# Performance work log

Measured on AMD Instinct MI355X. Metric: run time of the kernel, lower is better.

Reference implementation:

```python
import jax, jax.numpy as jnp
import numpy as np

INPUT_DIM = 256
RNN_DIM = 256
T, B = 1024, 64


def setup_inputs() -> dict:
    key = jax.random.key(0)
    ks = jax.random.split(key, 12)
    stdv = 1.0 / np.sqrt(RNN_DIM)
    u = lambda k, shape: jax.random.uniform(k, shape, jnp.float32, -stdv, stdv)
    return {
        "input_vectors": jax.random.normal(ks[0], (T, B, INPUT_DIM), jnp.float32),
        "W": u(ks[1], (INPUT_DIM, RNN_DIM)),
        "U": u(ks[2], (RNN_DIM, RNN_DIM)),
        "b": u(ks[3], (1, RNN_DIM)),
        "W_r": u(ks[4], (INPUT_DIM, RNN_DIM)),
        "U_r": u(ks[5], (RNN_DIM, RNN_DIM)),
        "b_r": u(ks[6], (1, RNN_DIM)),
        "W_z": u(ks[7], (INPUT_DIM, RNN_DIM)),
        "U_z": u(ks[8], (RNN_DIM, RNN_DIM)),
        "b_z": u(ks[9], (1, RNN_DIM)),
        "init_hidden": u(ks[10], (1, RNN_DIM)),
    }


def reference(input_vectors, W, U, b, W_r, U_r, b_r, W_z, U_z, b_z, init_hidden):
    # direction='l'. NOTE: the original module appends prev_hidden BEFORE the
    # update, so output[t] is the hidden state entering step t (output[0] is
    # the learned init). Also note the (nonstandard) combine uses (1-r), not
    # (1-z) \u2014 replicated faithfully.
    batch = input_vectors.shape[1]
    h0 = jnp.broadcast_to(init_hidden, (batch, RNN_DIM))

    def step(h, x):  # x: [B, input_dim], h: [B, rnn_dim]
        z = jax.nn.sigmoid(x @ W_z + h @ U_z + b_z)
        r = jax.nn.sigmoid(x @ W_r + h @ U_r + b_r)
        h_bar = jnp.tanh(x @ W + (r * h) @ U + b)
        new_h = (1.0 - r) * h + z * h_bar
        return new_h, h  # emit pre-update hidden, matching the torch code

    _, seq_hidden = jax.lax.scan(step, h0, input_vectors)
    return seq_hidden  # [T, B, rnn_dim]
```

## Files before the change

### kernel.cpp

```cpp
#include <hip/hip_runtime.h>
#include <hip/hip_bf16.h>

typedef __bf16 bf16x8 __attribute__((ext_vector_type(8)));
typedef __bf16 bf16x4 __attribute__((ext_vector_type(4)));
typedef float  f32x4  __attribute__((ext_vector_type(4)));
typedef unsigned int u32x4 __attribute__((ext_vector_type(4)));

#define T_STEPS 1024
#define LOG2E 1.4426950408889634f

#define LDS_BARRIER() asm volatile("s_waitcnt lgkmcnt(0)\n\ts_barrier" ::: "memory")

__device__ __forceinline__ float fast_sigmoid(float x) {
  float e = __builtin_amdgcn_exp2f(x * -LOG2E);
  return __builtin_amdgcn_rcpf(1.f + e);
}
__device__ __forceinline__ float fast_tanh(float x) {
  float e = __builtin_amdgcn_exp2f(x * (2.f * LOG2E));
  return 1.f - 2.f * __builtin_amdgcn_rcpf(1.f + e);
}
__device__ __forceinline__ float bf_lo(unsigned int u) { return __uint_as_float(u << 16); }
__device__ __forceinline__ float bf_hi(unsigned int u) { return __uint_as_float(u & 0xFFFF0000u); }


__global__ __launch_bounds__(256) void prep_frags(
    const float* __restrict__ Wz, const float* __restrict__ Wr, const float* __restrict__ Wh,
    const float* __restrict__ Uz, const float* __restrict__ Ur, const float* __restrict__ Uh,
    __bf16* __restrict__ afrag)
{
  int idx  = blockIdx.x * 256 + threadIdx.x;
  int mat  = idx >> 16;
  int cb   = (idx >> 12) & 15;
  int kblk = (idx >> 9) & 7;
  int l    = (idx >> 3) & 63;
  int j    = idx & 7;
  int k    = kblk * 32 + (l >> 4) * 8 + j;
  int col  = cb * 16 + (l & 15);
  const float* s = (mat == 0) ? Wz : (mat == 1) ? Wr : (mat == 2) ? Wh
                 : (mat == 3) ? Uz : (mat == 4) ? Ur : Uh;
  afrag[idx] = (__bf16)s[k * 256 + col];
}

__global__ __launch_bounds__(256) void gemm_x(
    const float* __restrict__ x, const __bf16* __restrict__ afrag,
    const float* __restrict__ bz, const float* __restrict__ br, const float* __restrict__ bh,
    __bf16* __restrict__ gates)
{
  int t = blockIdx.x;
  int tid = threadIdx.x;
  int l = tid & 63, w = tid >> 6;
  int q = l >> 4, m15 = l & 15;

  bf16x8 bfr[4][8];
#pragma unroll
  for (int g = 0; g < 4; g++) {
    const float* xrow = x + ((size_t)t * 64 + g * 16 + m15) * 256 + q * 8;
#pragma unroll
    for (int kb = 0; kb < 8; kb++) {
      f32x4 lo = *(const f32x4*)(xrow + kb * 32);
      f32x4 hi = *(const f32x4*)(xrow + kb * 32 + 4);
      bf16x8 v;
#pragma unroll
      for (int j = 0; j < 4; j++) { v[j] = (__bf16)lo[j]; v[4 + j] = (__bf16)hi[j]; }
      bfr[g][kb] = v;
    }
  }

  const bf16x8* af = (const bf16x8*)afrag;
#pragma unroll 1
  for (int jj = 0; jj < 12; jj++) {
    int nt = w + 4 * jj;
    int mat = nt >> 4, cb = nt & 15;
    f32x4 acc[4];
#pragma unroll
    for (int g = 0; g < 4; g++) acc[g] = (f32x4){0.f, 0.f, 0.f, 0.f};
#pragma unroll
    for (int kb = 0; kb < 8; kb++) {
      bf16x8 a = af[(nt * 8 + kb) * 64 + l];
#pragma unroll
      for (int g = 0; g < 4; g++)
        acc[g] = __builtin_amdgcn_mfma_f32_16x16x32_bf16(a, bfr[g][kb], acc[g], 0, 0, 0);
    }
    const float* bias = (mat == 0) ? bz : (mat == 1) ? br : bh;
    float b4[4];
#pragma unroll
    for (int i = 0; i < 4; i++) b4[i] = bias[cb * 16 + q * 4 + i];
    int p = cb >> 1, c = cb & 1;
#pragma unroll
    for (int g = 0; g < 4; g++) {
      bf16x4 ov;
#pragma unroll
      for (int i = 0; i < 4; i++) ov[i] = (__bf16)(acc[g][i] + b4[i]);
      *(bf16x4*)(gates + ((size_t)t * 4 + g) * 12288 + ((mat * 8 + p) * 64 + l) * 8 + c * 4) = ov;
    }
  }
}

__global__ __launch_bounds__(512, 2) void gru_rec(
    const __bf16* __restrict__ afrag, const __bf16* __restrict__ gates,
    const float* __restrict__ h0, float* __restrict__ out)
{
  __shared__ bf16x8 hfrag[512];
  __shared__ bf16x8 rhfrag[512];
  int g = blockIdx.x;
  int tid = threadIdx.x;
  int l = tid & 63, w = tid >> 6;
  int q = l >> 4, m15 = l & 15;

  bf16x8 wz[2][8], wr[2][8], wu[2][8];
  const bf16x8* af = (const bf16x8*)afrag;
#pragma unroll
  for (int c = 0; c < 2; c++) {
    int cbg = 2 * w + c;
#pragma unroll
    for (int kb = 0; kb < 8; kb++) {
      wz[c][kb] = af[((3 * 16 + cbg) * 8 + kb) * 64 + l];
      wr[c][kb] = af[((4 * 16 + cbg) * 8 + kb) * 64 + l];
      wu[c][kb] = af[((5 * 16 + cbg) * 8 + kb) * 64 + l];
    }
  }

  float hreg[2][4];
#pragma unroll
  for (int c = 0; c < 2; c++)
#pragma unroll
    for (int i = 0; i < 4; i++)
      hreg[c][i] = h0[32 * w + 16 * c + 4 * q + i];

  {
    const float* hp = h0 + w * 32 + q * 8;
    bf16x8 hv;
#pragma unroll
    for (int j = 0; j < 8; j++) hv[j] = (__bf16)hp[j];
    hfrag[w * 64 + l] = hv;
  }
  LDS_BARRIER();

  int wr0 = w * 128 + (m15 + 16 * (0 + (q >> 1))) * 2 + (q & 1);
  int wr1 = w * 128 + (m15 + 16 * (2 + (q >> 1))) * 2 + (q & 1);
  bf16x4* hf4  = (bf16x4*)hfrag;
  bf16x4* rhf4 = (bf16x4*)rhfrag;

  const int GSTRIDE = 4 * 12288;
  const __bf16* gt_p = gates + (size_t)g * 12288;
  int go_z = ((0 * 8 + w) * 64 + l) * 8;
  int go_r = ((1 * 8 + w) * 64 + l) * 8;
  int go_h = ((2 * 8 + w) * 64 + l) * 8;
  const float* out_t = out;
  int oo = (g * 16 + m15) * 256 + 32 * w + 4 * q;

  u32x4 nzu = *(const u32x4*)(gt_p + go_z);
  u32x4 nru = *(const u32x4*)(gt_p + go_r);

#pragma unroll 1
  for (int t = 0; t < T_STEPS; t++) {
    u32x4 ghu = *(const u32x4*)(gt_p + go_h);

    {
      f32x4 o0 = {hreg[0][0], hreg[0][1], hreg[0][2], hreg[0][3]};
      f32x4 o1 = {hreg[1][0], hreg[1][1], hreg[1][2], hreg[1][3]};
      *(f32x4*)(out_t + oo)      = o0;
      *(f32x4*)(out_t + oo + 16) = o1;
      out_t += 64 * 256;
    }

    f32x4 az0 = {bf_lo(nzu.x), bf_hi(nzu.x), bf_lo(nzu.y), bf_hi(nzu.y)};
    f32x4 az1 = {bf_lo(nzu.z), bf_hi(nzu.z), bf_lo(nzu.w), bf_hi(nzu.w)};
    f32x4 ar0 = {bf_lo(nru.x), bf_hi(nru.x), bf_lo(nru.y), bf_hi(nru.y)};
    f32x4 ar1 = {bf_lo(nru.z), bf_hi(nru.z), bf_lo(nru.w), bf_hi(nru.w)};
#pragma unroll
    for (int kb = 0; kb < 8; kb++) {
      bf16x8 hb = hfrag[kb * 64 + l];
      az0 = __builtin_amdgcn_mfma_f32_16x16x32_bf16(wz[0][kb], hb, az0, 0, 0, 0);
      az1 = __builtin_amdgcn_mfma_f32_16x16x32_bf16(wz[1][kb], hb, az1, 0, 0, 0);
      ar0 = __builtin_amdgcn_mfma_f32_16x16x32_bf16(wr[0][kb], hb, ar0, 0, 0, 0);
      ar1 = __builtin_amdgcn_mfma_f32_16x16x32_bf16(wr[1][kb], hb, ar1, 0, 0, 0);
    }
    float rhf[2][4];
    bf16x4 zb0, zb1, rhb0, rhb1;
#pragma unroll
    for (int i = 0; i < 4; i++) {
      float z0 = fast_sigmoid(az0[i]);
      float z1 = fast_sigmoid(az1[i]);
      float r0 = fast_sigmoid(ar0[i]);
      float r1 = fast_sigmoid(ar1[i]);
      zb0[i] = (__bf16)z0; zb1[i] = (__bf16)z1;
      rhf[0][i] = r0 * hreg[0][i];
      rhf[1][i] = r1 * hreg[1][i];
      rhb0[i] = (__bf16)rhf[0][i];
      rhb1[i] = (__bf16)rhf[1][i];
    }
    rhf4[wr0] = rhb0;
    rhf4[wr1] = rhb1;

    const __bf16* gn_p = gt_p + ((t < T_STEPS - 1) ? GSTRIDE : 0);
    nzu = *(const u32x4*)(gn_p + go_z);
    nru = *(const u32x4*)(gn_p + go_r);
    gt_p = gn_p;
    LDS_BARRIER();

    f32x4 ah0 = {bf_lo(ghu.x), bf_hi(ghu.x), bf_lo(ghu.y), bf_hi(ghu.y)};
    f32x4 ah1 = {bf_lo(ghu.z), bf_hi(ghu.z), bf_lo(ghu.w), bf_hi(ghu.w)};
#pragma unroll
    for (int kb = 0; kb < 8; kb++) {
      bf16x8 rb = rhfrag[kb * 64 + l];
      ah0 = __builtin_amdgcn_mfma_f32_16x16x32_bf16(wu[0][kb], rb, ah0, 0, 0, 0);
      ah1 = __builtin_amdgcn_mfma_f32_16x16x32_bf16(wu[1][kb], rb, ah1, 0, 0, 0);
    }
    bf16x4 nh0, nh1;
#pragma unroll
    for (int i = 0; i < 4; i++) {
      float hb0 = fast_tanh(ah0[i]);
      float hb1 = fast_tanh(ah1[i]);
      float z0 = (float)zb0[i], z1 = (float)zb1[i];
      hreg[0][i] = (hreg[0][i] - rhf[0][i]) + z0 * hb0;
      hreg[1][i] = (hreg[1][i] - rhf[1][i]) + z1 * hb1;
      nh0[i] = (__bf16)hreg[0][i];
      nh1[i] = (__bf16)hreg[1][i];
    }
    hf4[wr0] = nh0;
    hf4[wr1] = nh1;
    LDS_BARRIER();
  }
}

extern "C" void kernel_launch(void* const* d_in, const int* in_sizes, int n_in,
                              void* d_out, int out_size, void* d_ws, size_t ws_size,
                              hipStream_t stream)
{
  const float* x  = (const float*)d_in[0];
  const float* Wh = (const float*)d_in[1];
  const float* Uh = (const float*)d_in[2];
  const float* bh = (const float*)d_in[3];
  const float* Wr = (const float*)d_in[4];
  const float* Ur = (const float*)d_in[5];
  const float* br = (const float*)d_in[6];
  const float* Wz = (const float*)d_in[7];
  const float* Uz = (const float*)d_in[8];
  const float* bz = (const float*)d_in[9];
  const float* h0 = (const float*)d_in[10];

  __bf16* afrag = (__bf16*)d_ws;
  __bf16* gates = (__bf16*)d_ws + 393216;
  if (ws_size < (size_t)(393216 + 50331648) * 2) return;

  prep_frags<<<1536, 256, 0, stream>>>(Wz, Wr, Wh, Uz, Ur, Uh, afrag);
  gemm_x<<<1024, 256, 0, stream>>>(x, afrag, bz, br, bh, gates);
  gru_rec<<<4, 512, 0, stream>>>(afrag, gates, h0, (float*)d_out);
}
```

Baseline: 1.833 ms.

## Split recurrent kernel across 16 waves with one column block each

The recurrent kernel now launches 1024 threads (16 waves) per batch group instead of 512, so each wave owns a single 16-column block and issues half as many MFMAs per step. The z/r weight fragments stay in registers, while the candidate-gate U weights are re-read from global memory (likely cached) every step to save registers. This shortens each wave's serial chain per timestep, at the cost of more waves joining each barrier and extra per-step weight loads.

```diff
diff --git a/kernel.cpp b/kernel.cpp
--- a/kernel.cpp
+++ b/kernel.cpp
@@ -5,6 +5,7 @@
 typedef __bf16 bf16x4 __attribute__((ext_vector_type(4)));
 typedef float  f32x4  __attribute__((ext_vector_type(4)));
 typedef unsigned int u32x4 __attribute__((ext_vector_type(4)));
+typedef unsigned int u32x2 __attribute__((ext_vector_type(2)));
 
 #define T_STEPS 1024
 #define LOG2E 1.4426950408889634f
@@ -96,7 +97,7 @@
   }
 }
 
-__global__ __launch_bounds__(512, 2) void gru_rec(
+__global__ __launch_bounds__(1024) void gru_rec(
     const __bf16* __restrict__ afrag, const __bf16* __restrict__ gates,
     const float* __restrict__ h0, float* __restrict__ out)
 {
@@ -107,119 +108,94 @@
   int l = tid & 63, w = tid >> 6;
   int q = l >> 4, m15 = l & 15;
 
-  bf16x8 wz[2][8], wr[2][8], wu[2][8];
+  bf16x8 wz[8], wr[8];
   const bf16x8* af = (const bf16x8*)afrag;
 #pragma unroll
-  for (int c = 0; c < 2; c++) {
-    int cbg = 2 * w + c;
-#pragma unroll
-    for (int kb = 0; kb < 8; kb++) {
-      wz[c][kb] = af[((3 * 16 + cbg) * 8 + kb) * 64 + l];
-      wr[c][kb] = af[((4 * 16 + cbg) * 8 + kb) * 64 + l];
-      wu[c][kb] = af[((5 * 16 + cbg) * 8 + kb) * 64 + l];
-    }
-  }
-
-  float hreg[2][4];
-#pragma unroll
-  for (int c = 0; c < 2; c++)
-#pragma unroll
-    for (int i = 0; i < 4; i++)
-      hreg[c][i] = h0[32 * w + 16 * c + 4 * q + i];
-
-  {
-    const float* hp = h0 + w * 32 + q * 8;
-    bf16x8 hv;
-#pragma unroll
-    for (int j = 0; j < 8; j++) hv[j] = (__bf16)hp[j];
-    hfrag[w * 64 + l] = hv;
-  }
-  LDS_BARRIER();
-
-  int wr0 = w * 128 + (m15 + 16 * (0 + (q >> 1))) * 2 + (q & 1);
-  int wr1 = w * 128 + (m15 + 16 * (2 + (q >> 1))) * 2 + (q & 1);
+  for (int kb = 0; kb < 8; kb++) {
+    wz[kb] = af[((3 * 16 + w) * 8 + kb) * 64 + l];
+    wr[kb] = af[((4 * 16 + w) * 8 + kb) * 64 + l];
+  }
+  const bf16x8* wup = af + ((size_t)(5 * 16 + w) * 8) * 64 + l;
+
+  f32x4 hreg = *(const f32x4*)(h0 + 16 * w + 4 * q);
+
+  int wrs = (w >> 1) * 128 + (m15 + 16 * (2 * (w & 1) + (q >> 1))) * 2 + (q & 1);
   bf16x4* hf4  = (bf16x4*)hfrag;
   bf16x4* rhf4 = (bf16x4*)rhfrag;
 
+  {
+    bf16x4 hv;
+#pragma unroll
+    for (int i = 0; i < 4; i++) hv[i] = (__bf16)hreg[i];
+    hf4[wrs] = hv;
+  }
+  LDS_BARRIER();
+
   const int GSTRIDE = 4 * 12288;
   const __bf16* gt_p = gates + (size_t)g * 12288;
-  int go_z = ((0 * 8 + w) * 64 + l) * 8;
-  int go_r = ((1 * 8 + w) * 64 + l) * 8;
-  int go_h = ((2 * 8 + w) * 64 + l) * 8;
+  int go_z = ((0 * 8 + (w >> 1)) * 64 + l) * 8 + (w & 1) * 4;
+  int go_r = go_z + 8 * 64 * 8;
+  int go_h = go_z + 2 * 8 * 64 * 8;
   const float* out_t = out;
-  int oo = (g * 16 + m15) * 256 + 32 * w + 4 * q;
-
-  u32x4 nzu = *(const u32x4*)(gt_p + go_z);
-  u32x4 nru = *(const u32x4*)(gt_p + go_r);
+  int oo = (g * 16 + m15) * 256 + 16 * w + 4 * q;
+
+  u32x2 nzu = *(const u32x2*)(gt_p + go_z);
+  u32x2 nru = *(const u32x2*)(gt_p + go_r);
 
 #pragma unroll 1
   for (int t = 0; t < T_STEPS; t++) {
-    u32x4 ghu = *(const u32x4*)(gt_p + go_h);
-
-    {
-      f32x4 o0 = {hreg[0][0], hreg[0][1], hreg[0][2], hreg[0][3]};
-      f32x4 o1 = {hreg[1][0], hreg[1][1], hreg[1][2], hreg[1][3]};
-      *(f32x4*)(out_t + oo)      = o0;
-      *(f32x4*)(out_t + oo + 16) = o1;
-      out_t += 64 * 256;
-    }
-
-    f32x4 az0 = {bf_lo(nzu.x), bf_hi(nzu.x), bf_lo(nzu.y), bf_hi(nzu.y)};
-    f32x4 az1 = {bf_lo(nzu.z), bf_hi(nzu.z), bf_lo(nzu.w), bf_hi(nzu.w)};
-    f32x4 ar0 = {bf_lo(nru.x), bf_hi(nru.x), bf_lo(nru.y), bf_hi(nru.y)};
-    f32x4 ar1 = {bf_lo(nru.z), bf_hi(nru.z), bf_lo(nru.w), bf_hi(nru.w)};
+    u32x2 ghu = *(const u32x2*)(gt_p + go_h);
+
+    *(f32x4*)(out_t + oo) = hreg;
+    out_t += 64 * 256;
+
+    f32x4 az = {bf_lo(nzu.x), bf_hi(nzu.x), bf_lo(nzu.y), bf_hi(nzu.y)};
+    f32x4 ar = {bf_lo(nru.x), bf_hi(nru.x), bf_lo(nru.y), bf_hi(nru.y)};
 #pragma unroll
     for (int kb = 0; kb < 8; kb++) {
       bf16x8 hb = hfrag[kb * 64 + l];
-      az0 = __builtin_amdgcn_mfma_f32_16x16x32_bf16(wz[0][kb], hb, az0, 0, 0, 0);
-      az1 = __builtin_amdgcn_mfma_f32_16x16x32_bf16(wz[1][kb], hb, az1, 0, 0, 0);
-      ar0 = __builtin_amdgcn_mfma_f32_16x16x32_bf16(wr[0][kb], hb, ar0, 0, 0, 0);
-      ar1 = __builtin_amdgcn_mfma_f32_16x16x32_bf16(wr[1][kb], hb, ar1, 0, 0, 0);
-    }
-    float rhf[2][4];
-    bf16x4 zb0, zb1, rhb0, rhb1;
+      az = __builtin_amdgcn_mfma_f32_16x16x32_bf16(wz[kb], hb, az, 0, 0, 0);
+      ar = __builtin_amdgcn_mfma_f32_16x16x32_bf16(wr[kb], hb, ar, 0, 0, 0);
+    }
+
+    bf16x8 wu[8];
+#pragma unroll
+    for (int kb = 0; kb < 8; kb++) wu[kb] = wup[kb * 64];
+
+    f32x4 hmr;
+    bf16x4 zb, rhb;
 #pragma unroll
     for (int i = 0; i < 4; i++) {
-      float z0 = fast_sigmoid(az0[i]);
-      float z1 = fast_sigmoid(az1[i]);
-      float r0 = fast_sigmoid(ar0[i]);
-      float r1 = fast_sigmoid(ar1[i]);
-      zb0[i] = (__bf16)z0; zb1[i] = (__bf16)z1;
-      rhf[0][i] = r0 * hreg[0][i];
-      rhf[1][i] = r1 * hreg[1][i];
-      rhb0[i] = (__bf16)rhf[0][i];
-      rhb1[i] = (__bf16)rhf[1][i];
-    }
-    rhf4[wr0] = rhb0;
-    rhf4[wr1] = rhb1;
+      float z = fast_sigmoid(az[i]);
+      float r = fast_sigmoid(ar[i]);
+      float rh = r * hreg[i];
+      zb[i]  = (__bf16)z;
+      rhb[i] = (__bf16)rh;
+      hmr[i] = hreg[i] - rh;
+    }
+    rhf4[wrs] = rhb;
 
     const __bf16* gn_p = gt_p + ((t < T_STEPS - 1) ? GSTRIDE : 0);
-    nzu = *(const u32x4*)(gn_p + go_z);
-    nru = *(const u32x4*)(gn_p + go_r);
+    nzu = *(const u32x2*)(gn_p + go_z);
+    nru = *(const u32x2*)(gn_p + go_r);
     gt_p = gn_p;
     LDS_BARRIER();
 
-    f32x4 ah0 = {bf_lo(ghu.x), bf_hi(ghu.x), bf_lo(ghu.y), bf_hi(ghu.y)};
-    f32x4 ah1 = {bf_lo(ghu.z), bf_hi(ghu.z), bf_lo(ghu.w), bf_hi(ghu.w)};
+    f32x4 ah = {bf_lo(ghu.x), bf_hi(ghu.x), bf_lo(ghu.y), bf_hi(ghu.y)};
 #pragma unroll
     for (int kb = 0; kb < 8; kb++) {
       bf16x8 rb = rhfrag[kb * 64 + l];
-      ah0 = __builtin_amdgcn_mfma_f32_16x16x32_bf16(wu[0][kb], rb, ah0, 0, 0, 0);
-      ah1 = __builtin_amdgcn_mfma_f32_16x16x32_bf16(wu[1][kb], rb, ah1, 0, 0, 0);
-    }
-    bf16x4 nh0, nh1;
+      ah = __builtin_amdgcn_mfma_f32_16x16x32_bf16(wu[kb], rb, ah, 0, 0, 0);
+    }
+    bf16x4 nh;
 #pragma unroll
     for (int i = 0; i < 4; i++) {
-      float hb0 = fast_tanh(ah0[i]);
-      float hb1 = fast_tanh(ah1[i]);
-      float z0 = (float)zb0[i], z1 = (float)zb1[i];
-      hreg[0][i] = (hreg[0][i] - rhf[0][i]) + z0 * hb0;
-      hreg[1][i] = (hreg[1][i] - rhf[1][i]) + z1 * hb1;
-      nh0[i] = (__bf16)hreg[0][i];
-      nh1[i] = (__bf16)hreg[1][i];
-    }
-    hf4[wr0] = nh0;
-    hf4[wr1] = nh1;
+      float hb = fast_tanh(ah[i]);
+      float z  = (float)zb[i];
+      hreg[i] = hmr[i] + z * hb;
+      nh[i] = (__bf16)hreg[i];
+    }
+    hf4[wrs] = nh;
     LDS_BARRIER();
   }
 }
@@ -246,5 +222,5 @@
 
   prep_frags<<<1536, 256, 0, stream>>>(Wz, Wr, Wh, Uz, Ur, Uh, afrag);
   gemm_x<<<1024, 256, 0, stream>>>(x, afrag, bz, br, bh, gates);
-  gru_rec<<<4, 512, 0, stream>>>(afrag, gates, h0, (float*)d_out);
-}
+  gru_rec<<<4, 1024, 0, stream>>>(afrag, gates, h0, (float*)d_out);
+}
```

Measured after the change: 2.297 ms. +25.4%, slower.

## Fuse input GEMM and GRU recurrence into one kernel with counter-based sync

Applied to the files above, without the earlier changes.

Merges the input-projection GEMM and the recurrent kernel into a single launch. The last four blocks run the recurrence and, every 16 timesteps, spin on per-chunk atomic counters that the GEMM blocks increment once their gate tiles are written. This lets the recurrence start while later gate chunks are still being computed, and it removes a kernel boundary. GEMM blocks now use 512 threads, and gate reads switch to nontemporal loads. The cost is polling overhead and possible contention between GEMM blocks and the latency-critical recurrent blocks on the same CUs.

```diff
diff --git a/kernel.cpp b/kernel.cpp
--- a/kernel.cpp
+++ b/kernel.cpp
@@ -11,6 +11,11 @@
 
 #define LDS_BARRIER() asm volatile("s_waitcnt lgkmcnt(0)\n\ts_barrier" ::: "memory")
 
+#define GPOLL(gg) \
+  while (__hip_atomic_load(&cnt[gg], __ATOMIC_ACQUIRE, __HIP_MEMORY_SCOPE_AGENT) < 16u || \
+         __hip_atomic_load(&cnt[(gg) + 1], __ATOMIC_ACQUIRE, __HIP_MEMORY_SCOPE_AGENT) < 16u) \
+    __builtin_amdgcn_s_sleep(2)
+
 __device__ __forceinline__ float fast_sigmoid(float x) {
   float e = __builtin_amdgcn_exp2f(x * -LOG2E);
   return __builtin_amdgcn_rcpf(1.f + e);
@@ -26,8 +31,10 @@
 __global__ __launch_bounds__(256) void prep_frags(
     const float* __restrict__ Wz, const float* __restrict__ Wr, const float* __restrict__ Wh,
     const float* __restrict__ Uz, const float* __restrict__ Ur, const float* __restrict__ Uh,
-    __bf16* __restrict__ afrag)
+    __bf16* __restrict__ afrag, unsigned* __restrict__ cnt)
 {
+  if (blockIdx.x == 0 && threadIdx.x < 65)
+    cnt[threadIdx.x] = (threadIdx.x == 64) ? 16u : 0u;
   int idx  = blockIdx.x * 256 + threadIdx.x;
   int mat  = idx >> 16;
   int cb   = (idx >> 12) & 15;
@@ -41,69 +48,75 @@
   afrag[idx] = (__bf16)s[k * 256 + col];
 }
 
-__global__ __launch_bounds__(256) void gemm_x(
+__global__ __launch_bounds__(512, 2) void fused(
     const float* __restrict__ x, const __bf16* __restrict__ afrag,
     const float* __restrict__ bz, const float* __restrict__ br, const float* __restrict__ bh,
-    __bf16* __restrict__ gates)
+    __bf16* __restrict__ gates, const float* __restrict__ h0,
+    float* __restrict__ out, unsigned* __restrict__ cnt)
 {
-  int t = blockIdx.x;
+  int bid = blockIdx.x;
   int tid = threadIdx.x;
-  int l = tid & 63, w = tid >> 6;
-  int q = l >> 4, m15 = l & 15;
-
-  bf16x8 bfr[4][8];
-#pragma unroll
-  for (int g = 0; g < 4; g++) {
-    const float* xrow = x + ((size_t)t * 64 + g * 16 + m15) * 256 + q * 8;
-#pragma unroll
-    for (int kb = 0; kb < 8; kb++) {
-      f32x4 lo = *(const f32x4*)(xrow + kb * 32);
-      f32x4 hi = *(const f32x4*)(xrow + kb * 32 + 4);
-      bf16x8 v;
-#pragma unroll
-      for (int j = 0; j < 4; j++) { v[j] = (__bf16)lo[j]; v[4 + j] = (__bf16)hi[j]; }
-      bfr[g][kb] = v;
-    }
-  }
-
-  const bf16x8* af = (const bf16x8*)afrag;
+
+  if (bid < 1024) {
+    int t = bid;
+    int l = tid & 63, w = tid >> 6;
+    int q = l >> 4, m15 = l & 15;
+
+    bf16x8 bfr[4][8];
+#pragma unroll
+    for (int bg = 0; bg < 4; bg++) {
+      const float* xrow = x + ((size_t)t * 64 + bg * 16 + m15) * 256 + q * 8;
+#pragma unroll
+      for (int kb = 0; kb < 8; kb++) {
+        f32x4 lo = *(const f32x4*)(xrow + kb * 32);
+        f32x4 hi = *(const f32x4*)(xrow + kb * 32 + 4);
+        bf16x8 v;
+#pragma unroll
+        for (int j = 0; j < 4; j++) { v[j] = (__bf16)lo[j]; v[4 + j] = (__bf16)hi[j]; }
+        bfr[bg][kb] = v;
+      }
+    }
+
+    const bf16x8* af = (const bf16x8*)afrag;
 #pragma unroll 1
-  for (int jj = 0; jj < 12; jj++) {
-    int nt = w + 4 * jj;
-    int mat = nt >> 4, cb = nt & 15;
-    f32x4 acc[4];
-#pragma unroll
-    for (int g = 0; g < 4; g++) acc[g] = (f32x4){0.f, 0.f, 0.f, 0.f};
-#pragma unroll
-    for (int kb = 0; kb < 8; kb++) {
-      bf16x8 a = af[(nt * 8 + kb) * 64 + l];
-#pragma unroll
-      for (int g = 0; g < 4; g++)
-        acc[g] = __builtin_amdgcn_mfma_f32_16x16x32_bf16(a, bfr[g][kb], acc[g], 0, 0, 0);
-    }
-    const float* bias = (mat == 0) ? bz : (mat == 1) ? br : bh;
-    float b4[4];
-#pragma unroll
-    for (int i = 0; i < 4; i++) b4[i] = bias[cb * 16 + q * 4 + i];
-    int p = cb >> 1, c = cb & 1;
-#pragma unroll
-    for (int g = 0; g < 4; g++) {
-      bf16x4 ov;
-#pragma unroll
-      for (int i = 0; i < 4; i++) ov[i] = (__bf16)(acc[g][i] + b4[i]);
-      *(bf16x4*)(gates + ((size_t)t * 4 + g) * 12288 + ((mat * 8 + p) * 64 + l) * 8 + c * 4) = ov;
-    }
-  }
-}
-
-__global__ __launch_bounds__(512, 2) void gru_rec(
-    const __bf16* __restrict__ afrag, const __bf16* __restrict__ gates,
-    const float* __restrict__ h0, float* __restrict__ out)
-{
+    for (int jj = 0; jj < 6; jj++) {
+      int nt = w + 8 * jj;
+      int mat = nt >> 4, cb = nt & 15;
+      f32x4 acc[4];
+#pragma unroll
+      for (int bg = 0; bg < 4; bg++) acc[bg] = (f32x4){0.f, 0.f, 0.f, 0.f};
+#pragma unroll
+      for (int kb = 0; kb < 8; kb++) {
+        bf16x8 a = af[(nt * 8 + kb) * 64 + l];
+#pragma unroll
+        for (int bg = 0; bg < 4; bg++)
+          acc[bg] = __builtin_amdgcn_mfma_f32_16x16x32_bf16(a, bfr[bg][kb], acc[bg], 0, 0, 0);
+      }
+      const float* bias = (mat == 0) ? bz : (mat == 1) ? br : bh;
+      float b4[4];
+#pragma unroll
+      for (int i = 0; i < 4; i++) b4[i] = bias[cb * 16 + q * 4 + i];
+      int p = cb >> 1, c = cb & 1;
+#pragma unroll
+      for (int bg = 0; bg < 4; bg++) {
+        bf16x4 ov;
+#pragma unroll
+        for (int i = 0; i < 4; i++) ov[i] = (__bf16)(acc[bg][i] + b4[i]);
+        *(bf16x4*)(gates + ((size_t)t * 4 + bg) * 12288 + ((mat * 8 + p) * 64 + l) * 8 + c * 4) = ov;
+      }
+    }
+
+    __syncthreads();
+    if (tid == 0) {
+      __threadfence();
+      __hip_atomic_fetch_add(&cnt[t >> 4], 1u, __ATOMIC_RELEASE, __HIP_MEMORY_SCOPE_AGENT);
+    }
+    return;
+  }
+
   __shared__ bf16x8 hfrag[512];
   __shared__ bf16x8 rhfrag[512];
-  int g = blockIdx.x;
-  int tid = threadIdx.x;
+  int g = bid - 1024;
   int l = tid & 63, w = tid >> 6;
   int q = l >> 4, m15 = l & 15;
 
@@ -149,12 +162,15 @@
   const float* out_t = out;
   int oo = (g * 16 + m15) * 256 + 32 * w + 4 * q;
 
-  u32x4 nzu = *(const u32x4*)(gt_p + go_z);
-  u32x4 nru = *(const u32x4*)(gt_p + go_r);
+  GPOLL(0);
+  u32x4 nzu = __builtin_nontemporal_load((const u32x4*)(gt_p + go_z));
+  u32x4 nru = __builtin_nontemporal_load((const u32x4*)(gt_p + go_r));
 
 #pragma unroll 1
   for (int t = 0; t < T_STEPS; t++) {
-    u32x4 ghu = *(const u32x4*)(gt_p + go_h);
+    if ((t & 15) == 0) { GPOLL(t >> 4); }
+
+    u32x4 ghu = __builtin_nontemporal_load((const u32x4*)(gt_p + go_h));
 
     {
       f32x4 o0 = {hreg[0][0], hreg[0][1], hreg[0][2], hreg[0][3]};
@@ -194,8 +210,8 @@
     rhf4[wr1] = rhb1;
 
     const __bf16* gn_p = gt_p + ((t < T_STEPS - 1) ? GSTRIDE : 0);
-    nzu = *(const u32x4*)(gn_p + go_z);
-    nru = *(const u32x4*)(gn_p + go_r);
+    nzu = __builtin_nontemporal_load((const u32x4*)(gn_p + go_z));
+    nru = __builtin_nontemporal_load((const u32x4*)(gn_p + go_r));
     gt_p = gn_p;
     LDS_BARRIER();
 
@@ -242,9 +258,10 @@
 
   __bf16* afrag = (__bf16*)d_ws;
   __bf16* gates = (__bf16*)d_ws + 393216;
-  if (ws_size < (size_t)(393216 + 50331648) * 2) return;
-
-  prep_frags<<<1536, 256, 0, stream>>>(Wz, Wr, Wh, Uz, Ur, Uh, afrag);
-  gemm_x<<<1024, 256, 0, stream>>>(x, afrag, bz, br, bh, gates);
-  gru_rec<<<4, 512, 0, stream>>>(afrag, gates, h0, (float*)d_out);
-}
+  size_t base = (size_t)(393216 + 50331648) * 2;
+  unsigned* cnt = (unsigned*)((char*)d_ws + base);
+  if (ws_size < base + 4096) return;
+
+  prep_frags<<<1536, 256, 0, stream>>>(Wz, Wr, Wh, Uz, Ur, Uh, afrag, cnt);
+  fused<<<1028, 512, 0, stream>>>(x, afrag, bz, br, bh, gates, h0, (float*)d_out, cnt);
+}
```

After: 2.061 ms. +12.5%, slower.
